# Optimization experiments

Measured on AMD Instinct MI355X. Metric: run time of the kernel, lower is better.

Reference implementation:

```python
import math
import jax, jax.numpy as jnp
import numpy as np

N_REP = 4      # n_heads / n_kv_heads
DIM = 4096     # n_heads * head_dim
NEG_INF = -1e9 # additive mask value for disallowed positions


def setup_inputs() -> dict:
    key = jax.random.key(0)
    k0, k1, k2 = jax.random.split(key, 3)
    B, S, H, KVH, D, MAX_S = 2, 2048, 32, 8, 128, 2048
    q = jax.random.normal(k0, (B, S, H, D), dtype=jnp.float32)
    k = jax.random.normal(k1, (B, KVH, S, D), dtype=jnp.float32)
    v = jax.random.normal(k2, (B, KVH, S, D), dtype=jnp.float32)
    cache_k = jnp.zeros((B, KVH, MAX_S, D), dtype=jnp.float32)
    cache_v = jnp.zeros((B, KVH, MAX_S, D), dtype=jnp.float32)
    # full causal additive mask, indexed by input_pos rows in forward
    causal = jnp.tril(jnp.ones((MAX_S, MAX_S), dtype=bool))
    mask = jnp.where(causal, 0.0, NEG_INF).astype(jnp.float32)
    input_pos = jnp.arange(S, dtype=jnp.int32)
    return {
        "input_pos": input_pos,
        "q": q,
        "k": k,
        "v": v,
        "bsz": B,
        "seqlen": S,
        "mask": mask,
        "cache_k": cache_k,
        "cache_v": cache_v,
    }


def reference(input_pos, q, k, v, bsz, seqlen, mask, cache_k, cache_v):
    # q: (b, s, H, d) -> (b, H, s, d)
    qh = jnp.transpose(q, (0, 2, 1, 3))
    # KV cache update: write k, v at input_pos, return full cache (b, KVH, MAX_S, d)
    ck = cache_k.at[:, :, input_pos, :].set(k)
    cv = cache_v.at[:, :, input_pos, :].set(v)
    # GQA: repeat each kv head n_rep times -> (b, H, MAX_S, d)
    kf = jnp.repeat(ck, N_REP, axis=1)
    vf = jnp.repeat(cv, N_REP, axis=1)
    scale = 1.0 / math.sqrt(qh.shape[-1])
    attn_mask = mask[input_pos]  # (s, MAX_S)
    # scores: (b, H, s, MAX_S)
    attn = jnp.einsum("bhsd,bhtd->bhst", qh, kf) * scale + attn_mask
    w = jax.nn.softmax(attn, axis=-1)
    y = jnp.einsum("bhst,bhtd->bhsd", w, vf)
    # (b, H, s, d) -> (b, s, H*d)
    return jnp.transpose(y, (0, 2, 1, 3)).reshape(bsz, seqlen, DIM)
```

## Files before the change

kernel.cpp:

```cpp
#include <hip/hip_runtime.h>
#include <hip/hip_bf16.h>

typedef __attribute__((ext_vector_type(8))) short bf16x8;
typedef __attribute__((ext_vector_type(4))) float f32x4;
typedef __attribute__((ext_vector_type(8))) float f32x8;
typedef __attribute__((ext_vector_type(2))) float f32x2;
typedef __attribute__((ext_vector_type(8))) __bf16 bfv8;
typedef __attribute__((ext_vector_type(4))) __bf16 bfv4;
typedef __attribute__((ext_vector_type(2))) __bf16 bfv2;
typedef __attribute__((ext_vector_type(2))) unsigned int u32x2;

#define B_ 2
#define S_ 2048
#define H_ 32
#define KVH_ 8
#define D_ 128
#define BM 128
#define BN 64
#define NQT (S_ / BM)
#define NQP (NQT / 2)

__device__ __forceinline__ bf16x8 cvt8(f32x8 v) {
    union { bfv8 b; bf16x8 s; } u;
    u.b = __builtin_convertvector(v, bfv8);
    return u.s;
}

#define GLD16(g, l) __builtin_amdgcn_global_load_lds(                     \
    (const __attribute__((address_space(1))) unsigned int*)(g),           \
    (__attribute__((address_space(3))) unsigned int*)(l), 16, 0, 0)

__global__ __launch_bounds__(256) void conv_k(const float* __restrict__ k,
                                              short* __restrict__ kws) {
    const int idx = (blockIdx.x * 256 + threadIdx.x) * 8;
    f32x8 a = *(const f32x8*)(k + idx);
    *(bf16x8*)(kws + idx) = cvt8(a);
}

__global__ __launch_bounds__(256) void conv_vt(const float* __restrict__ v,
                                               short* __restrict__ vws) {
    __shared__ short tl[64 * 68];
    const int d0 = blockIdx.x * 64;
    const int t0 = blockIdx.y * 64;
    const int z  = blockIdx.z;
    const int tid = threadIdx.x;
    const float* vb = v + (size_t)z * S_ * D_;
    short* wb = vws + (size_t)z * D_ * S_;
    #pragma unroll
    for (int i = 0; i < 4; ++i) {
        const int chunk = i * 256 + tid;
        const int tr = chunk >> 4;
        const int c4 = (chunk & 15) << 2;
        float4 f = *(const float4*)(vb + (t0 + tr) * D_ + d0 + c4);
        union { bfv4 b; ushort4 s; } u;
        u.b = __builtin_convertvector((f32x4){f.x, f.y, f.z, f.w}, bfv4);
        *(ushort4*)(&tl[tr * 68 + c4]) = u.s;
    }
    __syncthreads();
    #pragma unroll
    for (int i = 0; i < 2; ++i) {
        const int chunk = i * 256 + tid;
        const int d = chunk >> 3;
        const int u8 = chunk & 7;
        bf16x8 r;
        #pragma unroll
        for (int w = 0; w < 8; ++w) {
            const int t = 2 * u8 + (w >> 2) + 16 * (w & 3);
            r[w] = tl[t * 68 + d];
        }
        *(bf16x8*)(wb + (size_t)(d0 + d) * S_ + t0 + u8 * 8) = r;
    }
}

#define STAGE(ti_, bufi_)  do {                                            \
    const short* kt2_ = kt + (ti_) * (BN * D_);                            \
    const short* vt2_ = vt + (ti_) * BN;                                   \
    short* kdst_ = &lds_k[bufi_][0];                                       \
    short* vdst_ = &lds_v[bufi_][0];                                       \
    _Pragma("unroll")                                                      \
    for (int rd_ = 0; rd_ < 4; ++rd_) {                                    \
        const int slot_ = rd_ * 256 + tid;                                 \
        const int r_  = slot_ >> 4;                                        \
        const int cg_ = (slot_ & 15) ^ (r_ & 7);                           \
        GLD16(kt2_ + r_ * D_ + cg_ * 8, kdst_ + (rd_ * 256 + wave * 64) * 8); \
    }                                                                      \
    _Pragma("unroll")                                                      \
    for (int rd_ = 0; rd_ < 4; ++rd_) {                                    \
        const int slot_ = rd_ * 256 + tid;                                 \
        const int d_  = slot_ >> 3;                                        \
        const int cg_ = (slot_ & 7) ^ (d_ & 7);                            \
        GLD16(vt2_ + (size_t)d_ * S_ + cg_ * 8, vdst_ + (rd_ * 256 + wave * 64) * 8); \
    }                                                                      \
} while (0)

__global__ __launch_bounds__(256, 2) void fa_fwd(
    const float* __restrict__ q, const short* __restrict__ kws,
    const short* __restrict__ vws, float* __restrict__ out)
{
    __shared__ short lds_k[2][64 * 128];
    __shared__ short lds_v[2][128 * 64];
    __shared__ short lds_p[4 * 16 * 64];

    const int flat = blockIdx.x + NQP * (blockIdx.y + H_ * blockIdx.z);
    const int xcd  = flat & 7;
    const int idx  = flat >> 3;
    const int work = xcd * 64 + idx;
    const int bkvh = work >> 5;
    const int rem  = work & 31;
    const int qp   = rem >> 2;
    const int b    = bkvh >> 3;
    const int kvh  = bkvh & 7;
    const int h    = (kvh << 2) | (rem & 3);

    const int tid  = threadIdx.x;
    const int wave = __builtin_amdgcn_readfirstlane(tid >> 6);
    const int lane = tid & 63;
    const int quad = lane >> 4;
    const int l16  = lane & 15;
    const int x7   = l16 & 7;

    const float sl2e = 0.08838834764831843f * 1.4426950408889634f;

    const short* kt = kws + (size_t)(b * KVH_ + kvh) * S_ * D_;
    const short* vt = vws + (size_t)(b * KVH_ + kvh) * D_ * S_;
    short* pw = lds_p + wave * 1024;

    #pragma unroll 1
    for (int phase = 0; phase < 2; ++phase) {
        const int qt = phase ? (NQT - 1 - qp) : qp;
        const int wr = qt * BM + wave * 32;
        const int nt = 2 * qt + 2;

        STAGE(0, 0);

        bf16x8 qf[2][4];
        #pragma unroll
        for (int mb = 0; mb < 2; ++mb) {
            const float* qrow = q + (size_t)((b * S_ + wr + mb * 16 + l16) * H_ + h) * D_;
            #pragma unroll
            for (int c = 0; c < 4; ++c) {
                f32x8 a = *(const f32x8*)(qrow + c * 32 + quad * 8);
                qf[mb][c] = cvt8(a * sl2e);
            }
        }

        f32x4 o[2][8];
        #pragma unroll
        for (int mb = 0; mb < 2; ++mb)
            #pragma unroll
            for (int db = 0; db < 8; ++db) o[mb][db] = (f32x4){0.f, 0.f, 0.f, 0.f};
        float Lr[2][4] = {{0.f,0.f,0.f,0.f},{0.f,0.f,0.f,0.f}};

        int bi = 0;
        for (int ti = 0; ti < nt; ++ti) {
            if (ti + 1 < nt) {
                STAGE(ti + 1, bi ^ 1);
                asm volatile("s_waitcnt vmcnt(8)" ::: "memory");
            } else {
                asm volatile("s_waitcnt vmcnt(0)" ::: "memory");
            }
            __builtin_amdgcn_s_barrier();
            __builtin_amdgcn_sched_barrier(0);

            const int t0 = ti * BN;
            if (t0 <= wr + 31) {
                const short* kb = &lds_k[bi][0];
                const short* vb = &lds_v[bi][0];

                f32x4 sc[2][4];
                #pragma unroll
                for (int mb = 0; mb < 2; ++mb)
                    #pragma unroll
                    for (int nb = 0; nb < 4; ++nb) sc[mb][nb] = (f32x4){0.f,0.f,0.f,0.f};
                __builtin_amdgcn_s_setprio(1);
                #pragma unroll
                for (int c = 0; c < 4; ++c) {
                    #pragma unroll
                    for (int nb = 0; nb < 4; ++nb) {
                        bf16x8 kf = *(const bf16x8*)(&kb[(nb * 16 + l16) * 128 +
                                                         (((c * 4 + quad) ^ x7) * 8)]);
                        sc[0][nb] = __builtin_amdgcn_mfma_f32_16x16x32_bf16(qf[0][c], kf, sc[0][nb], 0, 0, 0);
                        sc[1][nb] = __builtin_amdgcn_mfma_f32_16x16x32_bf16(qf[1][c], kf, sc[1][nb], 0, 0, 0);
                    }
                }
                __builtin_amdgcn_s_setprio(0);

                const bool needmask = (t0 + BN - 1 > wr);
                if (needmask) {
                    #pragma unroll
                    for (int mb = 0; mb < 2; ++mb)
                        #pragma unroll
                        for (int nb = 0; nb < 4; ++nb)
                            #pragma unroll
                            for (int r = 0; r < 4; ++r) {
                                const int tcol = t0 + nb * 16 + l16;
                                const int srow = wr + mb * 16 + quad * 4 + r;
                                if (tcol > srow) sc[mb][nb][r] = -1e30f;
                            }
                }
                #pragma unroll
                for (int mb = 0; mb < 2; ++mb)
                    #pragma unroll
                    for (int nb = 0; nb < 4; ++nb)
                        #pragma unroll
                        for (int r = 0; r < 4; ++r)
                            sc[mb][nb][r] = exp2f(sc[mb][nb][r]);
                #pragma unroll
                for (int mb = 0; mb < 2; ++mb)
                    #pragma unroll
                    for (int r = 0; r < 4; ++r)
                        Lr[mb][r] += (sc[mb][0][r] + sc[mb][1][r]) + (sc[mb][2][r] + sc[mb][3][r]);

                bf16x8 pf[2][2];
                #pragma unroll
                for (int mb = 0; mb < 2; ++mb) {
                    #pragma unroll
                    for (int r = 0; r < 4; ++r) {
                        const int rw = quad * 4 + r;
                        union { bfv2 b; unsigned u; } p0, p1;
                        p0.b = __builtin_convertvector((f32x2){sc[mb][0][r], sc[mb][1][r]}, bfv2);
                        p1.b = __builtin_convertvector((f32x2){sc[mb][2][r], sc[mb][3][r]}, bfv2);
                        *(u32x2*)(&pw[rw * 64 + (((l16 >> 1) ^ (rw & 7)) * 8) + (l16 & 1) * 4]) =
                            (u32x2){p0.u, p1.u};
                    }
                    #pragma unroll
                    for (int kk = 0; kk < 2; ++kk)
                        pf[mb][kk] = *(const bf16x8*)(&pw[l16 * 64 +
                                                         (((kk * 4 + quad) ^ x7) * 8)]);
                }

                __builtin_amdgcn_s_setprio(1);
                #pragma unroll
                for (int kk = 0; kk < 2; ++kk) {
                    #pragma unroll
                    for (int db = 0; db < 8; ++db) {
                        bf16x8 vf = *(const bf16x8*)(&vb[(db * 16 + l16) * 64 +
                                                         (((kk * 4 + quad) ^ x7) * 8)]);
                        o[0][db] = __builtin_amdgcn_mfma_f32_16x16x32_bf16(pf[0][kk], vf, o[0][db], 0, 0, 0);
                        o[1][db] = __builtin_amdgcn_mfma_f32_16x16x32_bf16(pf[1][kk], vf, o[1][db], 0, 0, 0);
                    }
                }
                __builtin_amdgcn_s_setprio(0);
            }

            __builtin_amdgcn_s_barrier();
            __builtin_amdgcn_sched_barrier(0);
            bi ^= 1;
        }

        #pragma unroll
        for (int mb = 0; mb < 2; ++mb)
            #pragma unroll
            for (int r = 0; r < 4; ++r) {
                float l = Lr[mb][r];
                l += __shfl_xor(l, 1, 16);
                l += __shfl_xor(l, 2, 16);
                l += __shfl_xor(l, 4, 16);
                l += __shfl_xor(l, 8, 16);
                Lr[mb][r] = 1.0f / l;
            }
        #pragma unroll
        for (int mb = 0; mb < 2; ++mb)
            #pragma unroll
            for (int r = 0; r < 4; ++r) {
                const int srow = wr + mb * 16 + quad * 4 + r;
                float* orow = out + (size_t)(b * S_ + srow) * (H_ * D_) + h * D_;
                #pragma unroll
                for (int db = 0; db < 8; ++db)
                    orow[db * 16 + l16] = o[mb][db][r] * Lr[mb][r];
            }
    }
}

extern "C" void kernel_launch(void* const* d_in, const int* in_sizes, int n_in,
                              void* d_out, int out_size, void* d_ws, size_t ws_size,
                              hipStream_t stream) {
    const float* q = (const float*)d_in[1];
    const float* k = (const float*)d_in[2];
    const float* v = (const float*)d_in[3];
    float* out = (float*)d_out;
    short* kws = (short*)d_ws;
    short* vws = kws + (size_t)B_ * KVH_ * S_ * D_;

    conv_k<<<(B_ * KVH_ * S_ * D_) / (256 * 8), 256, 0, stream>>>(k, kws);
    conv_vt<<<dim3(D_ / 64, S_ / 64, B_ * KVH_), 256, 0, stream>>>(v, vws);
    fa_fwd<<<dim3(NQP, H_, B_), 256, 0, stream>>>(q, kws, vws, out);
}
```

Measured before the change: 257.6 us.

## Load V fragments directly from global memory into registers instead of LDS staging

Drops the double-buffered LDS staging of V tiles and has each wave read its PV-MMA V fragments straight from global memory into registers. The loads are issued before and after the QK^T MMAs so their latency overlaps that compute. This halves LDS traffic and LDS footprint, which may allow higher occupancy. In exchange the four waves of a block each re-read the same V tile from global/L2, register pressure rises by 16 bf16x8 fragments, and the load latency is exposed within each iteration.

```diff
diff --git a/kernel.cpp b/kernel.cpp
--- a/kernel.cpp
+++ b/kernel.cpp
@@ -72,11 +72,9 @@
     }
 }
 
-#define STAGE(ti_, bufi_)  do {                                            \
+#define STAGEK(ti_, bufi_)  do {                                           \
     const short* kt2_ = kt + (ti_) * (BN * D_);                            \
-    const short* vt2_ = vt + (ti_) * BN;                                   \
     short* kdst_ = &lds_k[bufi_][0];                                       \
-    short* vdst_ = &lds_v[bufi_][0];                                       \
     _Pragma("unroll")                                                      \
     for (int rd_ = 0; rd_ < 4; ++rd_) {                                    \
         const int slot_ = rd_ * 256 + tid;                                 \
@@ -84,13 +82,6 @@
         const int cg_ = (slot_ & 15) ^ (r_ & 7);                           \
         GLD16(kt2_ + r_ * D_ + cg_ * 8, kdst_ + (rd_ * 256 + wave * 64) * 8); \
     }                                                                      \
-    _Pragma("unroll")                                                      \
-    for (int rd_ = 0; rd_ < 4; ++rd_) {                                    \
-        const int slot_ = rd_ * 256 + tid;                                 \
-        const int d_  = slot_ >> 3;                                        \
-        const int cg_ = (slot_ & 7) ^ (d_ & 7);                            \
-        GLD16(vt2_ + (size_t)d_ * S_ + cg_ * 8, vdst_ + (rd_ * 256 + wave * 64) * 8); \
-    }                                                                      \
 } while (0)
 
 __global__ __launch_bounds__(256, 2) void fa_fwd(
@@ -98,7 +89,6 @@
     const short* __restrict__ vws, float* __restrict__ out)
 {
     __shared__ short lds_k[2][64 * 128];
-    __shared__ short lds_v[2][128 * 64];
     __shared__ short lds_p[4 * 16 * 64];
 
     const int flat = blockIdx.x + NQP * (blockIdx.y + H_ * blockIdx.z);
@@ -131,7 +121,7 @@
         const int wr = qt * BM + wave * 32;
         const int nt = 2 * qt + 2;
 
-        STAGE(0, 0);
+        STAGEK(0, 0);
 
         bf16x8 qf[2][4];
         #pragma unroll
@@ -154,8 +144,8 @@
         int bi = 0;
         for (int ti = 0; ti < nt; ++ti) {
             if (ti + 1 < nt) {
-                STAGE(ti + 1, bi ^ 1);
-                asm volatile("s_waitcnt vmcnt(8)" ::: "memory");
+                STAGEK(ti + 1, bi ^ 1);
+                asm volatile("s_waitcnt vmcnt(4)" ::: "memory");
             } else {
                 asm volatile("s_waitcnt vmcnt(0)" ::: "memory");
             }
@@ -165,7 +155,12 @@
             const int t0 = ti * BN;
             if (t0 <= wr + 31) {
                 const short* kb = &lds_k[bi][0];
-                const short* vb = &lds_v[bi][0];
+                const short* vrow = vt + t0;
+
+                bf16x8 vf0[8], vf1[8];
+                #pragma unroll
+                for (int db = 0; db < 8; ++db)
+                    vf0[db] = *(const bf16x8*)(vrow + (size_t)(db * 16 + l16) * S_ + quad * 8);
 
                 f32x4 sc[2][4];
                 #pragma unroll
@@ -184,6 +179,10 @@
                     }
                 }
                 __builtin_amdgcn_s_setprio(0);
+
+                #pragma unroll
+                for (int db = 0; db < 8; ++db)
+                    vf1[db] = *(const bf16x8*)(vrow + (size_t)(db * 16 + l16) * S_ + 32 + quad * 8);
 
                 const bool needmask = (t0 + BN - 1 > wr);
                 if (needmask) {
@@ -231,14 +230,14 @@
 
                 __builtin_amdgcn_s_setprio(1);
                 #pragma unroll
-                for (int kk = 0; kk < 2; ++kk) {
-                    #pragma unroll
-                    for (int db = 0; db < 8; ++db) {
-                        bf16x8 vf = *(const bf16x8*)(&vb[(db * 16 + l16) * 64 +
-                                                         (((kk * 4 + quad) ^ x7) * 8)]);
-                        o[0][db] = __builtin_amdgcn_mfma_f32_16x16x32_bf16(pf[0][kk], vf, o[0][db], 0, 0, 0);
-                        o[1][db] = __builtin_amdgcn_mfma_f32_16x16x32_bf16(pf[1][kk], vf, o[1][db], 0, 0, 0);
-                    }
+                for (int db = 0; db < 8; ++db) {
+                    o[0][db] = __builtin_amdgcn_mfma_f32_16x16x32_bf16(pf[0][0], vf0[db], o[0][db], 0, 0, 0);
+                    o[1][db] = __builtin_amdgcn_mfma_f32_16x16x32_bf16(pf[1][0], vf0[db], o[1][db], 0, 0, 0);
+                }
+                #pragma unroll
+                for (int db = 0; db < 8; ++db) {
+                    o[0][db] = __builtin_amdgcn_mfma_f32_16x16x32_bf16(pf[0][1], vf1[db], o[0][db], 0, 0, 0);
+                    o[1][db] = __builtin_amdgcn_mfma_f32_16x16x32_bf16(pf[1][1], vf1[db], o[1][db], 0, 0, 0);
                 }
                 __builtin_amdgcn_s_setprio(0);
             }
```

New measurement: 325.1 us. 1.26x slower.
